# Kernel tuning notes

Hardware: AMD Instinct MI355X
Metric: run time of the kernel (lower is better)

Reference implementation:

```python
import jax, jax.numpy as jnp
import numpy as np

N_HEAD = 8
LINEAR_DIM = 64
IN_PIXELS = 4096  # h*w = 64*64
D = N_HEAD * LINEAR_DIM  # 512
C = 128
LN_EPS = 1e-6
BN_EPS = 1e-5


def setup_inputs() -> dict:
    key = jax.random.key(0)
    ks = jax.random.split(key, 10)
    shp = (16, C, 64, 64)
    # Kaiming-uniform-ish small init for weights (torch Linear weight layout: [out, in])
    def lin(k, out_f, in_f):
        lim = 1.0 / np.sqrt(in_f)
        return jax.random.uniform(k, (out_f, in_f), jnp.float32, -lim, lim)
    return {
        "v": jax.random.normal(ks[0], shp, jnp.float32),
        "k": jax.random.normal(ks[1], shp, jnp.float32),
        "q": jax.random.normal(ks[2], shp, jnp.float32),
        "w_qs": lin(ks[3], D, IN_PIXELS),
        "w_ks": lin(ks[4], D, IN_PIXELS),
        "w_vs": lin(ks[5], D, IN_PIXELS),
        "w_fc": lin(ks[6], IN_PIXELS, D),
        "ln_gamma": jnp.ones((D,), jnp.float32),
        "ln_beta": jnp.zeros((D,), jnp.float32),
        "temperature": jnp.asarray(IN_PIXELS ** 0.5, jnp.float32),
        "bn_gamma": jnp.ones((C,), jnp.float32),
        "bn_beta": jnp.zeros((C,), jnp.float32),
    }


def _layer_norm(x, gamma, beta):
    # torch-faithful: unbiased std (ddof=1), divide by (std + eps)
    mean = jnp.mean(x, axis=-1, keepdims=True)
    var = jnp.var(x, axis=-1, keepdims=True, ddof=1)
    std = jnp.sqrt(var)
    return gamma * (x - mean) / (std + LN_EPS) + beta


def reference(v, k, q, w_qs, w_ks, w_vs, w_fc, ln_gamma, ln_beta, temperature, bn_gamma, bn_beta):
    b, c, h, w = q.shape
    P = h * w
    qf = q.reshape(b, c, P)
    kf = k.reshape(b, c, P)
    vf = v.reshape(b, c, P)
    residual = vf
    # QKV projections: [b,c,P] @ W^T -> [b,c,D] -> [b,nh,c,ld]
    def proj(x, W):
        y = jnp.einsum('bcp,dp->bcd', x, W)
        return y.reshape(b, c, N_HEAD, LINEAR_DIM).transpose(0, 2, 1, 3)
    Q = proj(qf, w_qs)
    K = proj(kf, w_ks)
    V = proj(vf, w_vs)
    # channel-wise attention: scores [b,nh,c,c]
    scores = jnp.einsum('bhcd,bhed->bhce', Q / temperature, K)
    attn = jax.nn.softmax(scores, axis=-1)
    O = jnp.einsum('bhce,bhed->bhcd', attn, V)
    O = O.transpose(0, 2, 1, 3).reshape(b, c, N_HEAD * LINEAR_DIM)
    # Swish -> LayerNorm -> fc -> residual
    O = O * jax.nn.sigmoid(O)
    O = _layer_norm(O, ln_gamma, ln_beta)
    O = jnp.einsum('bcd,pd->bcp', O, w_fc)
    out = (residual + O).reshape(b, c, h, w)
    # BatchNorm2d in training mode: batch stats over (b,h,w), biased variance
    mean = jnp.mean(out, axis=(0, 2, 3), keepdims=True)
    var = jnp.var(out, axis=(0, 2, 3), keepdims=True)
    out = (out - mean) / jnp.sqrt(var + BN_EPS)
    out = out * bn_gamma[None, :, None, None] + bn_beta[None, :, None, None]
    return out
```

## Files before the change

### kernel.cpp

```cpp
#include <hip/hip_runtime.h>
#include <hip/hip_bf16.h>
#include <stdint.h>

typedef __attribute__((ext_vector_type(8))) short bf16x8;
typedef __attribute__((ext_vector_type(4))) float f32x4;

#define AS1(p) ((const __attribute__((address_space(1))) uint32_t*)(p))
#define AS3(p) ((__attribute__((address_space(3))) uint32_t*)(p))

#define VM12   asm volatile("s_waitcnt vmcnt(12)")
#define VM0    asm volatile("s_waitcnt vmcnt(0)")
#define LG0    asm volatile("s_waitcnt lgkmcnt(0)")
#define SBAR   __builtin_amdgcn_s_barrier()
#define SCHED0 __builtin_amdgcn_sched_barrier(0)

__device__ __forceinline__ ushort f2bf(float f) {
  uint32_t u = __float_as_uint(f);
  uint32_t r = (u + 0x7fffu + ((u >> 16) & 1u)) >> 16;
  return (ushort)r;
}

__device__ __forceinline__ float bf2f(ushort u) {
  uint32_t v = ((uint32_t)u) << 16;
  return __uint_as_float(v);
}

__device__ __forceinline__ uint4 cvt8u(float4 a0, float4 a1) {
  uint4 r;
  asm("v_cvt_pk_bf16_f32 %0, %1, %2" : "=v"(r.x) : "v"(a0.x), "v"(a0.y));
  asm("v_cvt_pk_bf16_f32 %0, %1, %2" : "=v"(r.y) : "v"(a0.z), "v"(a0.w));
  asm("v_cvt_pk_bf16_f32 %0, %1, %2" : "=v"(r.z) : "v"(a1.x), "v"(a1.y));
  asm("v_cvt_pk_bf16_f32 %0, %1, %2" : "=v"(r.w) : "v"(a1.z), "v"(a1.w));
  return r;
}

__global__ __launch_bounds__(256) void pack4(
    const float* __restrict__ s0, const float* __restrict__ s1,
    const float* __restrict__ s2, const float* __restrict__ s3,
    ushort* __restrict__ o0, ushort* __restrict__ o1,
    ushort* __restrict__ o2, ushort* __restrict__ o3, int n)
{
  const float* s; ushort* o;
  switch (blockIdx.y) {
    case 0: s = s0; o = o0; break;
    case 1: s = s1; o = o1; break;
    case 2: s = s2; o = o2; break;
    default: s = s3; o = o3; break;
  }
  int stride = gridDim.x * 1024;
  for (int i = (blockIdx.x * 256 + threadIdx.x) * 4; i < n; i += stride) {
    float4 v = *(const float4*)(s + i);
    ushort4 u;
    u.x = f2bf(v.x); u.y = f2bf(v.y); u.z = f2bf(v.z); u.w = f2bf(v.w);
    *(ushort4*)(o + i) = u;
  }
}

__global__ __launch_bounds__(256, 3) void gemm_qkv(
    const float* __restrict__ aq, const float* __restrict__ ak, const float* __restrict__ av,
    const ushort* __restrict__ wq, const ushort* __restrict__ wk, const ushort* __restrict__ wv,
    ushort* __restrict__ part, int lgs)
{
  __shared__ __align__(16) ushort At[128 * 64];
  __shared__ __align__(16) ushort Bt[2][128 * 64];
  int per = gridDim.x >> 3;
  int bid = blockIdx.x;
  int swz = (bid & 7) * per + (bid >> 3);
  int y = swz & 3, x = (swz >> 2) & 15, zz = swz >> 6;
  int g = zz >> lgs, s = zz & ((1 << lgs) - 1);
  const float* A; const ushort* Bm;
  if (g == 0)      { A = aq; Bm = wq; }
  else if (g == 1) { A = ak; Bm = wk; }
  else             { A = av; Bm = wv; }
  ushort* Pd = part + ((size_t)zz) * 1048576;
  const int K = 4096;
  const int kchunk = K >> lgs;
  const int k0 = s * kchunk, kend = k0 + kchunk;
  int rowBase = x * 128;
  int colBase = y * 128;
  int tid = threadIdx.x, l = tid & 63, w = tid >> 6;
  int wr = w >> 1, wc = w & 1, fr = l & 15, fq = l >> 4;

  int arow = tid >> 3;
  int aslot = tid & 7;
  int aswz = aslot ^ (arow & 7);
  const float* Abase = A + (size_t)(rowBase + arow) * K + aslot * 8;
  char* At0 = (char*)At + arow * 128 + aswz * 16;

  f32x4 acc[4][4];
#pragma unroll
  for (int m = 0; m < 4; ++m)
#pragma unroll
    for (int n = 0; n < 4; ++n) acc[m][n] = (f32x4){0.f, 0.f, 0.f, 0.f};

  float4 a0, a1, a2, a3, a4, a5, a6, a7;

#define LOADA(ktn) do { \
    a0 = *(const float4*)(Abase + (size_t)0 * K + (ktn)); \
    a1 = *(const float4*)(Abase + (size_t)0 * K + (ktn) + 4); \
    a2 = *(const float4*)(Abase + (size_t)32 * K + (ktn)); \
    a3 = *(const float4*)(Abase + (size_t)32 * K + (ktn) + 4); \
    a4 = *(const float4*)(Abase + (size_t)64 * K + (ktn)); \
    a5 = *(const float4*)(Abase + (size_t)64 * K + (ktn) + 4); \
    a6 = *(const float4*)(Abase + (size_t)96 * K + (ktn)); \
    a7 = *(const float4*)(Abase + (size_t)96 * K + (ktn) + 4); \
  } while (0)

#define CVTWRITEA do { \
    *(uint4*)(At0 + 0 * 4096)  = cvt8u(a0, a1); \
    *(uint4*)(At0 + 1 * 4096)  = cvt8u(a2, a3); \
    *(uint4*)(At0 + 2 * 4096)  = cvt8u(a4, a5); \
    *(uint4*)(At0 + 3 * 4096)  = cvt8u(a6, a7); \
  } while (0)

#define STAGEB(bufIdx, ktn) do { \
    char* Bbuf_ = (char*)Bt[bufIdx]; \
    _Pragma("unroll") \
    for (int j = 0; j < 4; ++j) { \
      int c = ((w * 4 + j) << 6) + l; \
      int row = c >> 3, slot = c & 7; \
      int srccol = (slot ^ (row & 7)) * 8; \
      __builtin_amdgcn_global_load_lds(AS1(Bm + (size_t)(colBase + row) * K + (ktn) + srccol), \
                                       AS3(Bbuf_ + c * 16), 16, 0, 0); \
    } \
  } while (0)

#define MFMAPHASE(bufIdx) do { \
    const char* Bbuf_ = (const char*)Bt[bufIdx]; \
    _Pragma("unroll") \
    for (int kc = 0; kc < 2; ++kc) { \
      bf16x8 af[4], bv[4]; \
      _Pragma("unroll") \
      for (int m = 0; m < 4; ++m) { \
        int r = wr * 64 + m * 16 + fr; \
        int sl = (kc * 4 + fq) ^ (fr & 7); \
        af[m] = *(const bf16x8*)((const char*)At + r * 128 + sl * 16); \
      } \
      _Pragma("unroll") \
      for (int n = 0; n < 4; ++n) { \
        int r = wc * 64 + n * 16 + fr; \
        int sl = (kc * 4 + fq) ^ (fr & 7); \
        bv[n] = *(const bf16x8*)(Bbuf_ + r * 128 + sl * 16); \
      } \
      _Pragma("unroll") \
      for (int m = 0; m < 4; ++m) \
        _Pragma("unroll") \
        for (int n = 0; n < 4; ++n) \
          acc[m][n] = __builtin_amdgcn_mfma_f32_16x16x32_bf16(af[m], bv[n], acc[m][n], 0, 0, 0); \
    } \
  } while (0)

  LOADA(k0);
  STAGEB(0, k0);
  CVTWRITEA;
  LG0; SCHED0;

  int buf = 0;
#pragma unroll 1
  for (int kt = k0; kt < kend; kt += 64) {
    bool more = (kt + 64) < kend;
    if (more) {
      LOADA(kt + 64);
      STAGEB(buf ^ 1, kt + 64);
      VM12; SCHED0;
    } else {
      VM0; SCHED0;
    }
    SBAR; SCHED0;
    MFMAPHASE(buf);
    SBAR;
    if (more) {
      CVTWRITEA;
      LG0; SCHED0;
    }
    buf ^= 1;
  }

#undef LOADA
#undef CVTWRITEA
#undef STAGEB
#undef MFMAPHASE

#pragma unroll
  for (int m = 0; m < 4; ++m)
#pragma unroll
    for (int n = 0; n < 4; ++n)
#pragma unroll
      for (int r = 0; r < 4; ++r) {
        int row = rowBase + wr * 64 + m * 16 + fq * 4 + r;
        int col = colBase + wc * 64 + n * 16 + fr;
        Pd[(size_t)row * 512 + col] = f2bf(acc[m][n][r]);
      }
}

__global__ __launch_bounds__(256) void reduce_qkv(
    const ushort* __restrict__ part, ushort* __restrict__ Qp, ushort* __restrict__ Kp,
    ushort* __restrict__ Vp, int lgs)
{
  int g = blockIdx.y;
  ushort* dst = g == 0 ? Qp : (g == 1 ? Kp : Vp);
  const ushort* p = part + (((size_t)g) << lgs) * 1048576;
  int i = (blockIdx.x * 256 + threadIdx.x) * 8;
  int splits = 1 << lgs;
  float accv[8];
  {
    bf16x8 v = *(const bf16x8*)(p + i);
#pragma unroll
    for (int j = 0; j < 8; ++j) accv[j] = bf2f((ushort)v[j]);
  }
  for (int s = 1; s < splits; ++s) {
    bf16x8 v = *(const bf16x8*)(p + (size_t)s * 1048576 + i);
#pragma unroll
    for (int j = 0; j < 8; ++j) accv[j] += bf2f((ushort)v[j]);
  }
  ushort u[8];
#pragma unroll
  for (int j = 0; j < 8; ++j) u[j] = f2bf(accv[j]);
  *(uint4*)(dst + i) = *(uint4*)u;
}

__global__ __launch_bounds__(256) void attn(
    const ushort* __restrict__ Qp, const ushort* __restrict__ Kp, const ushort* __restrict__ Vp,
    float* __restrict__ Obuf, const float* __restrict__ temp)
{
  __shared__ __align__(16) ushort Qs[64 * 64];
  __shared__ __align__(16) ushort Ks[128 * 64];
  __shared__ __align__(16) ushort Vt[64 * 128];
  __shared__ __align__(16) float  Sl[64 * 128];
  __shared__ __align__(16) ushort Pl[64 * 128];
  __shared__ float rsum[64];
  int bh = blockIdx.y, b = bh >> 3, h = bh & 7;
  int c0 = blockIdx.x * 64;
  int tid = threadIdx.x, l = tid & 63, w = tid >> 6;
  int wr = w >> 1, wc = w & 1, fr = l & 15, fq = l >> 4;
  float invT = 1.0f / temp[0];
  const size_t rowQ = (size_t)(b * 128 + c0);

#pragma unroll
  for (int j = 0; j < 2; ++j) {
    int c = ((w * 2 + j) << 6) + l, row = c >> 3, cc = c & 7;
    __builtin_amdgcn_global_load_lds(AS1(Qp + (rowQ + row) * 512 + h * 64 + cc * 8),
                                     AS3((char*)Qs + (w * 2 + j) * 1024), 16, 0, 0);
  }
#pragma unroll
  for (int j = 0; j < 4; ++j) {
    int c = ((w * 4 + j) << 6) + l, row = c >> 3, cc = c & 7;
    __builtin_amdgcn_global_load_lds(AS1(Kp + (size_t)(b * 128 + row) * 512 + h * 64 + cc * 8),
                                     AS3((char*)Ks + (w * 4 + j) * 1024), 16, 0, 0);
  }
#pragma unroll
  for (int t = 0; t < 4; ++t) {
    int ch = tid + t * 256, e = ch >> 3, d0 = (ch & 7) * 8;
    bf16x8 vv = *(const bf16x8*)(Vp + (size_t)(b * 128 + e) * 512 + h * 64 + d0);
#pragma unroll
    for (int j = 0; j < 8; ++j) Vt[(d0 + j) * 128 + e] = (ushort)vv[j];
  }
  __syncthreads();

  f32x4 sa[2][4];
#pragma unroll
  for (int m = 0; m < 2; ++m)
#pragma unroll
    for (int n = 0; n < 4; ++n) sa[m][n] = (f32x4){0.f, 0.f, 0.f, 0.f};
#pragma unroll
  for (int kc = 0; kc < 2; ++kc) {
    bf16x8 aQ[2], bK[4];
#pragma unroll
    for (int m = 0; m < 2; ++m)
      aQ[m] = *(const bf16x8*)&Qs[(wr * 32 + m * 16 + fr) * 64 + kc * 32 + fq * 8];
#pragma unroll
    for (int n = 0; n < 4; ++n)
      bK[n] = *(const bf16x8*)&Ks[(wc * 64 + n * 16 + fr) * 64 + kc * 32 + fq * 8];
#pragma unroll
    for (int m = 0; m < 2; ++m)
#pragma unroll
      for (int n = 0; n < 4; ++n)
        sa[m][n] = __builtin_amdgcn_mfma_f32_16x16x32_bf16(aQ[m], bK[n], sa[m][n], 0, 0, 0);
  }
#pragma unroll
  for (int m = 0; m < 2; ++m)
#pragma unroll
    for (int n = 0; n < 4; ++n)
#pragma unroll
      for (int r = 0; r < 4; ++r)
        Sl[(wr * 32 + m * 16 + fq * 4 + r) * 128 + wc * 64 + n * 16 + fr] = sa[m][n][r] * invT;
  __syncthreads();

  {
    int row = tid >> 2, qq = tid & 3;
    const float* srow = Sl + row * 128 + qq * 32;
    float4 va[8];
#pragma unroll
    for (int i = 0; i < 8; ++i) va[i] = *(const float4*)(srow + i * 4);
    float mx = -1e30f;
#pragma unroll
    for (int i = 0; i < 8; ++i)
      mx = fmaxf(mx, fmaxf(fmaxf(va[i].x, va[i].y), fmaxf(va[i].z, va[i].w)));
    mx = fmaxf(mx, __shfl_xor(mx, 1));
    mx = fmaxf(mx, __shfl_xor(mx, 2));
    float ssum = 0.f;
    ushort* prow = Pl + row * 128 + qq * 32;
#pragma unroll
    for (int i = 0; i < 8; ++i) {
      float e0 = __expf(va[i].x - mx), e1 = __expf(va[i].y - mx);
      float e2 = __expf(va[i].z - mx), e3 = __expf(va[i].w - mx);
      ssum += (e0 + e1) + (e2 + e3);
      ushort4 u; u.x = f2bf(e0); u.y = f2bf(e1); u.z = f2bf(e2); u.w = f2bf(e3);
      *(ushort4*)(prow + i * 4) = u;
    }
    ssum += __shfl_xor(ssum, 1);
    ssum += __shfl_xor(ssum, 2);
    if (qq == 0) rsum[row] = ssum;
  }
  __syncthreads();

  f32x4 oa[2][2];
#pragma unroll
  for (int m = 0; m < 2; ++m)
#pragma unroll
    for (int n = 0; n < 2; ++n) oa[m][n] = (f32x4){0.f, 0.f, 0.f, 0.f};
#pragma unroll
  for (int kc = 0; kc < 4; ++kc) {
    bf16x8 aP[2], bV[2];
#pragma unroll
    for (int m = 0; m < 2; ++m)
      aP[m] = *(const bf16x8*)&Pl[(wr * 32 + m * 16 + fr) * 128 + kc * 32 + fq * 8];
#pragma unroll
    for (int n = 0; n < 2; ++n)
      bV[n] = *(const bf16x8*)&Vt[(wc * 32 + n * 16 + fr) * 128 + kc * 32 + fq * 8];
#pragma unroll
    for (int m = 0; m < 2; ++m)
#pragma unroll
      for (int n = 0; n < 2; ++n)
        oa[m][n] = __builtin_amdgcn_mfma_f32_16x16x32_bf16(aP[m], bV[n], oa[m][n], 0, 0, 0);
  }
#pragma unroll
  for (int m = 0; m < 2; ++m)
#pragma unroll
    for (int n = 0; n < 2; ++n)
#pragma unroll
      for (int r = 0; r < 4; ++r) {
        int row = wr * 32 + m * 16 + fq * 4 + r, col = wc * 32 + n * 16 + fr;
        Obuf[(rowQ + row) * 512 + h * 64 + col] = oa[m][n][r] / rsum[row];
      }
}

__global__ __launch_bounds__(256) void swish_ln(
    const float* __restrict__ O, ushort* __restrict__ X,
    const float* __restrict__ gamma, const float* __restrict__ beta)
{
  int row = blockIdx.x * 4 + (threadIdx.x >> 6);
  int lane = threadIdx.x & 63;
  const float* x = O + (size_t)row * 512 + lane * 8;
  float4 va = *(const float4*)(x);
  float4 vb = *(const float4*)(x + 4);
  float y[8] = {va.x, va.y, va.z, va.w, vb.x, vb.y, vb.z, vb.w};
  float s = 0.f, sq = 0.f;
#pragma unroll
  for (int i = 0; i < 8; ++i) {
    y[i] = y[i] / (1.f + __expf(-y[i]));
    s += y[i]; sq += y[i] * y[i];
  }
#pragma unroll
  for (int o = 1; o < 64; o <<= 1) { s += __shfl_xor(s, o); sq += __shfl_xor(sq, o); }
  float mean = s * (1.f / 512.f);
  float var = (sq - s * mean) * (1.f / 511.f);
  float inv = 1.f / (sqrtf(var) + 1e-6f);
  const float4 g0 = *(const float4*)(gamma + lane * 8);
  const float4 g1 = *(const float4*)(gamma + lane * 8 + 4);
  const float4 b0 = *(const float4*)(beta + lane * 8);
  const float4 b1 = *(const float4*)(beta + lane * 8 + 4);
  float gg[8] = {g0.x, g0.y, g0.z, g0.w, g1.x, g1.y, g1.z, g1.w};
  float bb[8] = {b0.x, b0.y, b0.z, b0.w, b1.x, b1.y, b1.z, b1.w};
  ushort u[8];
#pragma unroll
  for (int i = 0; i < 8; ++i) u[i] = f2bf(gg[i] * (y[i] - mean) * inv + bb[i]);
  *(uint4*)(X + (size_t)row * 512 + lane * 8) = *(uint4*)u;
}

__global__ __launch_bounds__(256) void gemm_fc(
    const ushort* __restrict__ A, const ushort* __restrict__ Bm,
    const float* __restrict__ resid, ushort* __restrict__ valb,
    float* __restrict__ bn_sum, float* __restrict__ bn_sq)
{
  __shared__ __align__(16) ushort At[128 * 64];
  __shared__ __align__(16) ushort Bt[128 * 64];
  __shared__ float csum[128], csq[128];
  const int K = 512;
  int rowBase = blockIdx.x * 128;
  int colBase = blockIdx.y * 128;
  int tid = threadIdx.x, l = tid & 63, w = tid >> 6;
  int wr = w >> 1, wc = w & 1, fr = l & 15, fq = l >> 4;
  if (tid < 128) { csum[tid] = 0.f; csq[tid] = 0.f; }
  f32x4 acc[4][4];
#pragma unroll
  for (int m = 0; m < 4; ++m)
#pragma unroll
    for (int n = 0; n < 4; ++n) acc[m][n] = (f32x4){0.f, 0.f, 0.f, 0.f};

  for (int kt = 0; kt < K; kt += 64) {
#pragma unroll
    for (int j = 0; j < 4; ++j) {
      int c = ((w * 4 + j) << 6) + l;
      int row = c >> 3, cc = c & 7;
      __builtin_amdgcn_global_load_lds(AS1(A + (size_t)(rowBase + row) * K + kt + cc * 8),
                                       AS3((char*)At + (w * 4 + j) * 1024), 16, 0, 0);
      __builtin_amdgcn_global_load_lds(AS1(Bm + (size_t)(colBase + row) * K + kt + cc * 8),
                                       AS3((char*)Bt + (w * 4 + j) * 1024), 16, 0, 0);
    }
    __syncthreads();
#pragma unroll
    for (int kc = 0; kc < 2; ++kc) {
      bf16x8 af[4], bfv[4];
#pragma unroll
      for (int m = 0; m < 4; ++m)
        af[m] = *(const bf16x8*)&At[(wr * 64 + m * 16 + fr) * 64 + kc * 32 + fq * 8];
#pragma unroll
      for (int n = 0; n < 4; ++n)
        bfv[n] = *(const bf16x8*)&Bt[(wc * 64 + n * 16 + fr) * 64 + kc * 32 + fq * 8];
#pragma unroll
      for (int m = 0; m < 4; ++m)
#pragma unroll
        for (int n = 0; n < 4; ++n)
          acc[m][n] = __builtin_amdgcn_mfma_f32_16x16x32_bf16(af[m], bfv[n], acc[m][n], 0, 0, 0);
    }
    __syncthreads();
  }
#pragma unroll
  for (int m = 0; m < 4; ++m)
#pragma unroll
    for (int r = 0; r < 4; ++r) {
      float ps = 0.f, pq = 0.f;
#pragma unroll
      for (int n = 0; n < 4; ++n) {
        int row = rowBase + wr * 64 + m * 16 + fq * 4 + r;
        int col = colBase + wc * 64 + n * 16 + fr;
        size_t idx = (size_t)row * 4096 + col;
        float val = acc[m][n][r] + resid[idx];
        valb[idx] = f2bf(val);
        ps += val; pq += val * val;
      }
#pragma unroll
      for (int o = 1; o < 16; o <<= 1) { ps += __shfl_xor(ps, o); pq += __shfl_xor(pq, o); }
      if (fr == 0) {
        int ch = wr * 64 + m * 16 + fq * 4 + r;
        atomicAdd(&csum[ch], ps);
        atomicAdd(&csq[ch], pq);
      }
    }
  __syncthreads();
  if (tid < 128) {
    atomicAdd(&bn_sum[tid], csum[tid]);
    atomicAdd(&bn_sq[tid], csq[tid]);
  }
}

__global__ __launch_bounds__(256) void bn_norm(
    const ushort* __restrict__ valb, float* __restrict__ out,
    const float* __restrict__ bn_sum, const float* __restrict__ bn_sq,
    const float* __restrict__ gamma, const float* __restrict__ beta)
{
  __shared__ float sc[128], sh[128];
  const float inv_n = 1.f / 65536.f;
  int tid = threadIdx.x;
  if (tid < 128) {
    float mean = bn_sum[tid] * inv_n;
    float var = bn_sq[tid] * inv_n - mean * mean;
    float g = gamma[tid] * rsqrtf(var + 1e-5f);
    sc[tid] = g;
    sh[tid] = beta[tid] - mean * g;
  }
  __syncthreads();
  int stride = gridDim.x * blockDim.x;
  for (int v = blockIdx.x * blockDim.x + tid; v < 1048576; v += stride) {
    int elem = v * 8;
    int ch = (elem >> 12) & 127;
    float g = sc[ch], bta = sh[ch];
    bf16x8 x = *(const bf16x8*)(valb + elem);
    float4 o0, o1;
    o0.x = bf2f((ushort)x[0]) * g + bta;
    o0.y = bf2f((ushort)x[1]) * g + bta;
    o0.z = bf2f((ushort)x[2]) * g + bta;
    o0.w = bf2f((ushort)x[3]) * g + bta;
    o1.x = bf2f((ushort)x[4]) * g + bta;
    o1.y = bf2f((ushort)x[5]) * g + bta;
    o1.z = bf2f((ushort)x[6]) * g + bta;
    o1.w = bf2f((ushort)x[7]) * g + bta;
    *(float4*)(out + elem) = o0;
    *(float4*)(out + elem + 4) = o1;
  }
}

extern "C" void kernel_launch(void* const* d_in, const int* in_sizes, int n_in,
                              void* d_out, int out_size, void* d_ws, size_t ws_size,
                              hipStream_t stream)
{
  const float* v_in = (const float*)d_in[0];
  const float* k_in = (const float*)d_in[1];
  const float* q_in = (const float*)d_in[2];
  const float* w_qs = (const float*)d_in[3];
  const float* w_ks = (const float*)d_in[4];
  const float* w_vs = (const float*)d_in[5];
  const float* w_fc = (const float*)d_in[6];
  const float* ln_g = (const float*)d_in[7];
  const float* ln_b = (const float*)d_in[8];
  const float* temp = (const float*)d_in[9];
  const float* bn_g = (const float*)d_in[10];
  const float* bn_b = (const float*)d_in[11];
  float* out = (float*)d_out;

  char* ws = (char*)d_ws;
  size_t off = 0;
  auto alloc = [&](size_t bytes) { char* p = ws + off; off += bytes; return p; };
  ushort* wq  = (ushort*)alloc(512ull * 4096 * 2);
  ushort* wk  = (ushort*)alloc(512ull * 4096 * 2);
  ushort* wv  = (ushort*)alloc(512ull * 4096 * 2);
  ushort* wfc = (ushort*)alloc(512ull * 4096 * 2);
  ushort* Qp  = (ushort*)alloc(2048ull * 512 * 2);
  ushort* Kp  = (ushort*)alloc(2048ull * 512 * 2);
  ushort* Vp  = (ushort*)alloc(2048ull * 512 * 2);
  float*  Obuf= (float*)alloc(2048ull * 512 * 4);
  ushort* X16 = (ushort*)alloc(2048ull * 512 * 2);
  ushort* valb= (ushort*)alloc(2048ull * 4096 * 2);
  float*  bns = (float*)alloc(128 * 4);
  float*  bnq = (float*)alloc(128 * 4);

  int lgs = 2;
  if (off + (3ull << lgs) * 1048576 * 2 > ws_size) lgs = 1;
  if (off + (3ull << lgs) * 1048576 * 2 > ws_size) lgs = 0;
  ushort* part = (ushort*)alloc((3ull << lgs) * 1048576 * 2);

  hipMemsetAsync(bns, 0, 256 * 4, stream);

  pack4<<<dim3(512, 4), 256, 0, stream>>>(w_qs, w_ks, w_vs, w_fc, wq, wk, wv, wfc,
                                          512 * 4096);
  gemm_qkv<<<16 * 4 * (3 << lgs), 256, 0, stream>>>(q_in, k_in, v_in, wq, wk, wv, part, lgs);
  reduce_qkv<<<dim3(512, 3), 256, 0, stream>>>(part, Qp, Kp, Vp, lgs);
  attn<<<dim3(2, 128), 256, 0, stream>>>(Qp, Kp, Vp, Obuf, temp);
  swish_ln<<<512, 256, 0, stream>>>(Obuf, X16, ln_g, ln_b);
  gemm_fc<<<dim3(16, 32), 256, 0, stream>>>(X16, wfc, v_in, valb, bns, bnq);
  bn_norm<<<2048, 256, 0, stream>>>(valb, out, bns, bnq, bn_g, bn_b);
}
```

Before: 114.8 us.

## Single-buffer QKV GEMM staging, raise occupancy, and deepen split-K

Drops the double-buffered B tile and the hand-written waitcnt/sched barriers in the QKV projection GEMM. It replaces them with a simple load, convert, sync, MFMA, sync loop, which cuts LDS use from 48KB to 32KB per block. Launch bounds rise from 3 to 5 blocks per CU, and split-K goes to 8 slices when workspace allows. The aim is to hide memory latency through occupancy and a larger grid instead of explicit software pipelining. This costs prefetch overlap within a block and doubles the partial-sum traffic for the reduce kernel.

```diff
diff --git a/kernel.cpp b/kernel.cpp
--- a/kernel.cpp
+++ b/kernel.cpp
@@ -7,12 +7,6 @@
 
 #define AS1(p) ((const __attribute__((address_space(1))) uint32_t*)(p))
 #define AS3(p) ((__attribute__((address_space(3))) uint32_t*)(p))
-
-#define VM12   asm volatile("s_waitcnt vmcnt(12)")
-#define VM0    asm volatile("s_waitcnt vmcnt(0)")
-#define LG0    asm volatile("s_waitcnt lgkmcnt(0)")
-#define SBAR   __builtin_amdgcn_s_barrier()
-#define SCHED0 __builtin_amdgcn_sched_barrier(0)
 
 __device__ __forceinline__ ushort f2bf(float f) {
   uint32_t u = __float_as_uint(f);
@@ -56,13 +50,13 @@
   }
 }
 
-__global__ __launch_bounds__(256, 3) void gemm_qkv(
+__global__ __launch_bounds__(256, 5) void gemm_qkv(
     const float* __restrict__ aq, const float* __restrict__ ak, const float* __restrict__ av,
     const ushort* __restrict__ wq, const ushort* __restrict__ wk, const ushort* __restrict__ wv,
     ushort* __restrict__ part, int lgs)
 {
   __shared__ __align__(16) ushort At[128 * 64];
-  __shared__ __align__(16) ushort Bt[2][128 * 64];
+  __shared__ __align__(16) ushort Bt[128 * 64];
   int per = gridDim.x >> 3;
   int bid = blockIdx.x;
   int swz = (bid & 7) * per + (bid >> 3);
@@ -113,20 +107,18 @@
     *(uint4*)(At0 + 3 * 4096)  = cvt8u(a6, a7); \
   } while (0)
 
-#define STAGEB(bufIdx, ktn) do { \
-    char* Bbuf_ = (char*)Bt[bufIdx]; \
+#define STAGEB(ktn) do { \
     _Pragma("unroll") \
     for (int j = 0; j < 4; ++j) { \
       int c = ((w * 4 + j) << 6) + l; \
       int row = c >> 3, slot = c & 7; \
       int srccol = (slot ^ (row & 7)) * 8; \
       __builtin_amdgcn_global_load_lds(AS1(Bm + (size_t)(colBase + row) * K + (ktn) + srccol), \
-                                       AS3(Bbuf_ + c * 16), 16, 0, 0); \
+                                       AS3((char*)Bt + c * 16), 16, 0, 0); \
     } \
   } while (0)
 
-#define MFMAPHASE(bufIdx) do { \
-    const char* Bbuf_ = (const char*)Bt[bufIdx]; \
+#define MFMAPHASE do { \
     _Pragma("unroll") \
     for (int kc = 0; kc < 2; ++kc) { \
       bf16x8 af[4], bv[4]; \
@@ -140,7 +132,7 @@
       for (int n = 0; n < 4; ++n) { \
         int r = wc * 64 + n * 16 + fr; \
         int sl = (kc * 4 + fq) ^ (fr & 7); \
-        bv[n] = *(const bf16x8*)(Bbuf_ + r * 128 + sl * 16); \
+        bv[n] = *(const bf16x8*)((const char*)Bt + r * 128 + sl * 16); \
       } \
       _Pragma("unroll") \
       for (int m = 0; m < 4; ++m) \
@@ -151,29 +143,18 @@
   } while (0)
 
   LOADA(k0);
-  STAGEB(0, k0);
-  CVTWRITEA;
-  LG0; SCHED0;
-
-  int buf = 0;
+  STAGEB(k0);
+
 #pragma unroll 1
   for (int kt = k0; kt < kend; kt += 64) {
-    bool more = (kt + 64) < kend;
-    if (more) {
+    CVTWRITEA;
+    __syncthreads();
+    MFMAPHASE;
+    __syncthreads();
+    if (kt + 64 < kend) {
       LOADA(kt + 64);
-      STAGEB(buf ^ 1, kt + 64);
-      VM12; SCHED0;
-    } else {
-      VM0; SCHED0;
+      STAGEB(kt + 64);
     }
-    SBAR; SCHED0;
-    MFMAPHASE(buf);
-    SBAR;
-    if (more) {
-      CVTWRITEA;
-      LG0; SCHED0;
-    }
-    buf ^= 1;
   }
 
 #undef LOADA
@@ -525,9 +506,8 @@
   float*  bns = (float*)alloc(128 * 4);
   float*  bnq = (float*)alloc(128 * 4);
 
-  int lgs = 2;
-  if (off + (3ull << lgs) * 1048576 * 2 > ws_size) lgs = 1;
-  if (off + (3ull << lgs) * 1048576 * 2 > ws_size) lgs = 0;
+  int lgs = 3;
+  while (lgs > 0 && off + (3ull << lgs) * 1048576 * 2 > ws_size) --lgs;
   ushort* part = (ushort*)alloc((3ull << lgs) * 1048576 * 2);
 
   hipMemsetAsync(bns, 0, 256 * 4, stream);
```

New measurement: 330.1 us. 2.88x slower.
